# Optimization experiments

Hardware: AMD Instinct MI355X
Metric: run time of the kernel (lower is better)

## Reference

```python
import jax, jax.numpy as jnp
import numpy as np

B, DIM1, DIM2, LATENT, T = 16, 1024, 1024, 512, 2048  # T == video_feat_dim
LN_EPS = 1e-5


def setup_inputs() -> dict:
    key = jax.random.key(0)
    ks = jax.random.split(key, 8)
    def xavier(k, shape):
        fan_out, fan_in = shape
        std = float(np.sqrt(2.0 / (fan_in + fan_out)))
        return jax.random.normal(k, shape, dtype=jnp.float32) * std
    return {
        "input1": jax.random.normal(ks[0], (B, DIM1, T), dtype=jnp.float32),
        "input2": jax.random.normal(ks[1], (B, DIM2, T), dtype=jnp.float32),
        "theta_w": xavier(ks[2], (LATENT, DIM2)),
        "theta_b": jnp.zeros((LATENT,), jnp.float32),
        "phi_w": xavier(ks[3], (LATENT, DIM1)),
        "phi_b": jnp.zeros((LATENT,), jnp.float32),
        "g_w": xavier(ks[4], (LATENT, DIM1)),
        "g_b": jnp.zeros((LATENT,), jnp.float32),
        "ln_gamma": jnp.ones((LATENT, T), jnp.float32),
        "ln_beta": jnp.zeros((LATENT, T), jnp.float32),
        "out_w": xavier(ks[5], (DIM2, LATENT)),
        "out_b": jnp.zeros((DIM2,), jnp.float32),
    }


def reference(input1, input2, theta_w, theta_b, phi_w, phi_b, g_w, g_b,
              ln_gamma, ln_beta, out_w, out_b):
    # 1x1 Conv1d == channel-wise matmul
    theta_x = jnp.einsum('ld,bdt->btl', theta_w, input2) + theta_b          # [B,T2,L]
    phi_x = jnp.einsum('ld,bdt->blt', phi_w, input1) + phi_b[:, None]       # [B,L,T1]
    scores = jnp.einsum('btl,bls->bts', theta_x, phi_x)                      # [B,T2,T1] (unscaled)
    p = jax.nn.softmax(scores, axis=-1)
    g_x = jnp.einsum('ld,bdt->btl', g_w, input1) + g_b                       # [B,T1,L]
    t_x = jnp.einsum('bts,bsl->blt', p, g_x)                                 # [B,L,T2]
    # LayerNorm over the last two dims jointly [LATENT, T]
    mu = jnp.mean(t_x, axis=(1, 2), keepdims=True)
    var = jnp.var(t_x, axis=(1, 2), keepdims=True)
    h = (t_x - mu) * jax.lax.rsqrt(var + LN_EPS) * ln_gamma + ln_beta
    h = jax.nn.relu(h)
    w_t = jnp.einsum('ol,blt->bot', out_w, h) + out_b[None, :, None]         # [B,DIM2,T2]
    return w_t + input2
```

## Files before the change

### kernel.cpp

```cpp
#include <hip/hip_runtime.h>
#include <hip/hip_bf16.h>

#define BB 16
#define D1 1024
#define D2 1024
#define LL 512
#define TT 2048
#define LN_EPS 1e-5f

typedef unsigned short u16;
typedef __attribute__((ext_vector_type(8))) _Float16 half8;
typedef __attribute__((ext_vector_type(4))) float f32x4;
typedef __attribute__((ext_vector_type(4))) unsigned int u32x4;

__device__ __forceinline__ u16 f2h(float v) {
    _Float16 h = (_Float16)v;
    return *(u16*)&h;
}
__device__ __forceinline__ float h2f(u16 u) {
    return (float)(*(const _Float16*)&u);
}

__device__ __forceinline__ void gload_lds16(const void* g, void* l) {
    __builtin_amdgcn_global_load_lds((const __attribute__((address_space(1))) void*)g,
                                     (__attribute__((address_space(3))) void*)l, 16, 0, 0);
}

#define MEMFENCE asm volatile("" ::: "memory")
__device__ __forceinline__ void block_barrier() {
    MEMFENCE; __builtin_amdgcn_s_barrier(); MEMFENCE;
}

template<int BIAS, int OMODE>
__global__ __launch_bounds__(512, 1) void nt_gemm(
    const u16* __restrict__ A, const u16* __restrict__ B,
    long sAb, long sBb, long sCb,
    int N, int Kd, int gx, int gy,
    const float* __restrict__ bias,
    void* __restrict__ out0,
    const float* __restrict__ resid, long sRb)
{
    __shared__ __align__(16) u16 smem[65536];

    const int nwg = gridDim.x;
    const int id = blockIdx.x;
    const int swz = (id & 7) * (nwg >> 3) + (id >> 3);
    const int bx = swz % gx;
    const int byz = swz / gx;
    const int by = byz % gy;
    const int b = byz / gy;

    const int tid = threadIdx.x;
    const long arow0 = (long)by * 256;
    const long brow0 = (long)bx * 256;
    const u16* Ab = A + (long)b * sAb + arow0 * Kd;
    const u16* Bb = B + (long)b * sBb + brow0 * Kd;

    const int wave = tid >> 6, lane = tid & 63;
    const int mh = wave >> 2;
    const int wm = mh * 128;
    const int wn = (wave & 3) * 64;
    const int lm = lane & 15, kg = lane >> 4;

    const int ntile = Kd >> 6;

    auto STAGE = [&](int buf, long k0) {
        u16* Ad = smem + buf * 32768;
        u16* Bd = Ad + 16384;
#pragma unroll
        for (int sw = 0; sw < 4; ++sw) {
            int idx = sw * 512 + tid;
            int m = idx >> 3, s = idx & 7;
            int gs = s ^ (m & 7);
            gload_lds16(Ab + k0 + (long)m * Kd + gs * 8, Ad + idx * 8);
        }
#pragma unroll
        for (int sw = 0; sw < 4; ++sw) {
            int idx = sw * 512 + tid;
            int m = idx >> 3, s = idx & 7;
            int gs = s ^ (m & 7);
            gload_lds16(Bb + k0 + (long)m * Kd + gs * 8, Bd + idx * 8);
        }
    };

    f32x4 acc[8][4];
#pragma unroll
    for (int i = 0; i < 8; ++i)
#pragma unroll
        for (int j = 0; j < 4; ++j) acc[i][j] = (f32x4){0.f, 0.f, 0.f, 0.f};

    STAGE(0, 0);
    if (ntile > 1) STAGE(1, 64);

    half8 a_[4][2], b_[2][2];

#define LOADA(ms_) do { \
    _Pragma("unroll") for (int f = 0; f < 4; ++f) \
    _Pragma("unroll") for (int kf = 0; kf < 2; ++kf) { \
        int mr = wm + (ms_) * 64 + f * 16 + lm; \
        int ss = (kf * 4 + kg) ^ (mr & 7); \
        a_[f][kf] = *(const half8*)(Ac + mr * 64 + ss * 8); } } while (0)
#define LOADB(ns_) do { \
    _Pragma("unroll") for (int f = 0; f < 2; ++f) \
    _Pragma("unroll") for (int kf = 0; kf < 2; ++kf) { \
        int nr = wn + (ns_) * 32 + f * 16 + lm; \
        int ss = (kf * 4 + kg) ^ (nr & 7); \
        b_[f][kf] = *(const half8*)(Bc + nr * 64 + ss * 8); } } while (0)
#define PH_MFMA(ms_, ns_) do { \
    block_barrier(); \
    asm volatile("s_waitcnt lgkmcnt(0)" ::: "memory"); \
    __builtin_amdgcn_sched_barrier(0); \
    __builtin_amdgcn_s_setprio(1); \
    _Pragma("unroll") for (int i = 0; i < 4; ++i) \
    _Pragma("unroll") for (int j = 0; j < 2; ++j) \
    _Pragma("unroll") for (int kf = 0; kf < 2; ++kf) \
        acc[(ms_) * 4 + i][(ns_) * 2 + j] = __builtin_amdgcn_mfma_f32_16x16x32_f16( \
            a_[i][kf], b_[j][kf], acc[(ms_) * 4 + i][(ns_) * 2 + j], 0, 0, 0); \
    __builtin_amdgcn_s_setprio(0); \
    block_barrier(); \
} while (0)

    for (int t = 0; t < ntile; ++t) {
        const int c = t & 1;
        const u16* Ac = smem + c * 32768;
        const u16* Bc = Ac + 16384;
        if (t + 1 < ntile) { asm volatile("s_waitcnt vmcnt(8)" ::: "memory"); }
        else               { asm volatile("s_waitcnt vmcnt(0)" ::: "memory"); }
        block_barrier();

        LOADA(0); LOADB(0); PH_MFMA(0, 0);
        LOADA(1);           PH_MFMA(1, 0);
        LOADB(1);           PH_MFMA(1, 1);
        LOADA(0);           PH_MFMA(0, 1);

        if (t + 2 < ntile) STAGE(c, (long)(t + 2) * 64);
    }
#undef LOADA
#undef LOADB
#undef PH_MFMA

    float* Cs = (float*)smem;
#pragma unroll
    for (int p = 0; p < 2; ++p) {
        __syncthreads();
        if (mh == p) {
#pragma unroll
            for (int ms = 0; ms < 2; ++ms)
#pragma unroll
                for (int i = 0; i < 4; ++i)
#pragma unroll
                    for (int ns = 0; ns < 2; ++ns)
#pragma unroll
                        for (int j = 0; j < 2; ++j)
#pragma unroll
                            for (int r = 0; r < 4; ++r) {
                                int row = ms * 64 + i * 16 + kg * 4 + r;
                                int col = wn + ns * 32 + j * 16 + lm;
                                Cs[row * 256 + (col ^ ((row & 7) << 2))] = acc[ms * 4 + i][ns * 2 + j][r];
                            }
        }
        __syncthreads();
        if (OMODE == 0 || OMODE == 3) {
#pragma unroll
            for (int it = 0; it < 16; ++it) {
                int elem = it * 512 + tid;
                int row = elem >> 6, c4 = elem & 63;
                int grow = (int)arow0 + p * 128 + row;
                int gcol = (int)brow0 + c4 * 4;
                f32x4 v = *(const f32x4*)&Cs[row * 256 + ((c4 ^ (row & 7)) << 2)];
                if (BIAS == 1) v += bias[grow];
                if (BIAS == 2) v += *(const f32x4*)(bias + gcol);
                long off = (long)b * sCb + (long)grow * N + gcol;
                if (OMODE == 3) {
                    f32x4 rv = __builtin_nontemporal_load(
                        (const f32x4*)(resid + (long)b * sRb + (long)grow * N + gcol));
                    v += rv;
                    __builtin_nontemporal_store(v, (f32x4*)((float*)out0 + off));
                } else {
                    *(f32x4*)((float*)out0 + off) = v;
                }
            }
        } else {
#pragma unroll
            for (int it = 0; it < 8; ++it) {
                int elem = it * 512 + tid;
                int row = elem >> 5, c8 = elem & 31;
                int grow = (int)arow0 + p * 128 + row;
                int gcol = (int)brow0 + c8 * 8;
                int g0 = (c8 * 2) ^ (row & 7);
                int g1 = (c8 * 2 + 1) ^ (row & 7);
                f32x4 u0 = *(const f32x4*)&Cs[row * 256 + g0 * 4];
                f32x4 u1 = *(const f32x4*)&Cs[row * 256 + g1 * 4];
                float vv[8] = {u0.x, u0.y, u0.z, u0.w, u1.x, u1.y, u1.z, u1.w};
                if (BIAS == 1) {
                    float bb = bias[grow];
#pragma unroll
                    for (int q = 0; q < 8; ++q) vv[q] += bb;
                }
                if (BIAS == 2) {
#pragma unroll
                    for (int q = 0; q < 8; ++q) vv[q] += bias[gcol + q];
                }
                union { u16 u[8]; u32x4 v4; } pk;
#pragma unroll
                for (int q = 0; q < 8; ++q) pk.u[q] = f2h(vv[q]);
                long off = (long)b * sCb + (long)grow * N + gcol;
                *(u32x4*)((u16*)out0 + off) = pk.v4;
            }
        }
    }
}

__device__ __forceinline__ void stage_tile_sm(const u16* __restrict__ g, int ldk, u16* lds, int tid) {
#pragma unroll
    for (int it = 0; it < 4; ++it) {
        int idx = it * 256 + tid;
        int m = idx >> 3, s = idx & 7;
        int gs = s ^ (m & 7);
        gload_lds16(g + (long)m * ldk + gs * 8, lds + idx * 8);
    }
}

template<int BIAS, int OMODE>
__global__ __launch_bounds__(256, 4) void nt_gemm_sm(
    const u16* __restrict__ A, const u16* __restrict__ B,
    long sAb, long sBb, long sCb,
    int N, int Kd, int gx, int gy,
    const float* __restrict__ bias,
    void* __restrict__ out0,
    const float* __restrict__ resid, long sRb)
{
    __shared__ __align__(16) u16 smem[2 * 128 * 64];
    u16* As = smem;
    u16* Bs = smem + 128 * 64;

    const int nwg = gridDim.x;
    const int id = blockIdx.x;
    const int swz = (id & 7) * (nwg >> 3) + (id >> 3);
    const int bx = swz % gx;
    const int byz = swz / gx;
    const int by = byz % gy;
    const int b = byz / gy;

    const int tid = threadIdx.x;
    const long arow0 = (long)by * 128;
    const long brow0 = (long)bx * 128;
    const u16* Ab = A + (long)b * sAb + arow0 * Kd;
    const u16* Bb = B + (long)b * sBb + brow0 * Kd;

    const int wave = tid >> 6, lane = tid & 63;
    const int wm = (wave >> 1) * 64, wn = (wave & 1) * 64;
    const int lm = lane & 15, kg = lane >> 4;

    f32x4 acc[4][4];
#pragma unroll
    for (int i = 0; i < 4; ++i)
#pragma unroll
        for (int j = 0; j < 4; ++j) acc[i][j] = (f32x4){0.f, 0.f, 0.f, 0.f};

    for (int k0 = 0; k0 < Kd; k0 += 64) {
        stage_tile_sm(Ab + k0, Kd, As, tid);
        stage_tile_sm(Bb + k0, Kd, Bs, tid);
        __syncthreads();
#pragma unroll
        for (int ks = 0; ks < 2; ++ks) {
            half8 af[4], bf[4];
#pragma unroll
            for (int f = 0; f < 4; ++f) {
                int mr = wm + f * 16 + lm;
                int as_ = (ks * 4 + kg) ^ (mr & 7);
                af[f] = *(const half8*)(As + mr * 64 + as_ * 8);
                int nr = wn + f * 16 + lm;
                int bs_ = (ks * 4 + kg) ^ (nr & 7);
                bf[f] = *(const half8*)(Bs + nr * 64 + bs_ * 8);
            }
#pragma unroll
            for (int i = 0; i < 4; ++i)
#pragma unroll
                for (int j = 0; j < 4; ++j)
                    acc[i][j] = __builtin_amdgcn_mfma_f32_16x16x32_f16(af[i], bf[j], acc[i][j], 0, 0, 0);
        }
        __syncthreads();
    }

    float* Cs = (float*)smem;
#pragma unroll
    for (int p = 0; p < 2; ++p) {
        if (p) __syncthreads();
        if (wm == p * 64) {
#pragma unroll
            for (int i = 0; i < 4; ++i)
#pragma unroll
                for (int j = 0; j < 4; ++j)
#pragma unroll
                    for (int r = 0; r < 4; ++r) {
                        int row = i * 16 + kg * 4 + r;
                        int col = wn + j * 16 + lm;
                        Cs[row * 128 + (col ^ ((row & 7) << 2))] = acc[i][j][r];
                    }
        }
        __syncthreads();
        if (OMODE == 0 || OMODE == 3) {
#pragma unroll
            for (int rr = 0; rr < 8; ++rr) {
                int elem = rr * 256 + tid;
                int row = elem >> 5, c4 = elem & 31;
                int grow = (int)arow0 + p * 64 + row;
                int gcol = (int)brow0 + c4 * 4;
                f32x4 v = *(const f32x4*)&Cs[row * 128 + ((c4 ^ (row & 7)) << 2)];
                if (BIAS == 1) v += bias[grow];
                if (BIAS == 2) v += *(const f32x4*)(bias + gcol);
                long off = (long)b * sCb + (long)grow * N + gcol;
                if (OMODE == 3) {
                    f32x4 rv = __builtin_nontemporal_load(
                        (const f32x4*)(resid + (long)b * sRb + (long)grow * N + gcol));
                    v += rv;
                    __builtin_nontemporal_store(v, (f32x4*)((float*)out0 + off));
                } else {
                    *(f32x4*)((float*)out0 + off) = v;
                }
            }
        } else {
#pragma unroll
            for (int rr = 0; rr < 4; ++rr) {
                int elem = rr * 256 + tid;
                int row = elem >> 4, c8 = elem & 15;
                int grow = (int)arow0 + p * 64 + row;
                int gcol = (int)brow0 + c8 * 8;
                int g0 = (c8 * 2) ^ (row & 7);
                int g1 = (c8 * 2 + 1) ^ (row & 7);
                f32x4 u0 = *(const f32x4*)&Cs[row * 128 + g0 * 4];
                f32x4 u1 = *(const f32x4*)&Cs[row * 128 + g1 * 4];
                float vv[8] = {u0.x, u0.y, u0.z, u0.w, u1.x, u1.y, u1.z, u1.w};
                if (BIAS == 1) {
                    float bb = bias[grow];
#pragma unroll
                    for (int q = 0; q < 8; ++q) vv[q] += bb;
                }
                if (BIAS == 2) {
#pragma unroll
                    for (int q = 0; q < 8; ++q) vv[q] += bias[gcol + q];
                }
                union { u16 u[8]; u32x4 v4; } pk;
#pragma unroll
                for (int q = 0; q < 8; ++q) pk.u[q] = f2h(vv[q]);
                long off = (long)b * sCb + (long)grow * N + gcol;
                *(u32x4*)((u16*)out0 + off) = pk.v4;
            }
        }
    }
}

__global__ __launch_bounds__(256) void transpose_h(const float* __restrict__ in,
                                                   u16* __restrict__ o16, int D, int T) {
    __shared__ float tile[64][65];
    int b = blockIdx.z;
    const float* src = in + (long)b * D * T;
    long obase = (long)b * D * T;
    int t0 = blockIdx.x * 64, d0 = blockIdx.y * 64;
    int tx = threadIdx.x & 63, ty = threadIdx.x >> 6;
#pragma unroll
    for (int i = 0; i < 64; i += 4)
        tile[ty + i][tx] = __builtin_nontemporal_load(&src[(long)(d0 + ty + i) * T + t0 + tx]);
    __syncthreads();
#pragma unroll
    for (int i = 0; i < 64; i += 4) {
        long o = obase + (long)(t0 + ty + i) * D + d0 + tx;
        o16[o] = f2h(tile[tx][ty + i]);
    }
}

__global__ __launch_bounds__(256) void transpose_f32(const float* __restrict__ in,
                                                     float* __restrict__ out, int R, int C) {
    __shared__ float tile[64][65];
    int c0 = blockIdx.x * 64, r0 = blockIdx.y * 64;
    int tx = threadIdx.x & 63, ty = threadIdx.x >> 6;
#pragma unroll
    for (int i = 0; i < 64; i += 4)
        tile[ty + i][tx] = in[(long)(r0 + ty + i) * C + c0 + tx];
    __syncthreads();
#pragma unroll
    for (int i = 0; i < 64; i += 4)
        out[(long)(c0 + ty + i) * R + r0 + tx] = tile[tx][ty + i];
}

__global__ __launch_bounds__(256) void conv_w(const float* __restrict__ w,
                                              u16* __restrict__ h, int n) {
    int i = blockIdx.x * 256 + threadIdx.x;
    if (i < n) h[i] = f2h(w[i]);
}

__global__ __launch_bounds__(256) void softmax_rows(const float* __restrict__ S, u16* __restrict__ P) {
    long row = (long)blockIdx.z * TT + blockIdx.x;
    const float* s = S + row * TT;
    u16* p = P + row * TT;
    int tid = threadIdx.x;
    f32x4 v0 = *(const f32x4*)(s + tid * 8);
    f32x4 v1 = *(const f32x4*)(s + tid * 8 + 4);
    float x[8] = {v0.x, v0.y, v0.z, v0.w, v1.x, v1.y, v1.z, v1.w};
    float m = x[0];
#pragma unroll
    for (int j = 1; j < 8; ++j) m = fmaxf(m, x[j]);
#pragma unroll
    for (int off = 32; off; off >>= 1) m = fmaxf(m, __shfl_xor(m, off, 64));
    __shared__ float red[8];
    int wave = tid >> 6, lane = tid & 63;
    if (lane == 0) red[wave] = m;
    __syncthreads();
    m = fmaxf(fmaxf(red[0], red[1]), fmaxf(red[2], red[3]));
    float e[8]; float sum = 0.f;
#pragma unroll
    for (int j = 0; j < 8; ++j) { e[j] = __expf(x[j] - m); sum += e[j]; }
#pragma unroll
    for (int off = 32; off; off >>= 1) sum += __shfl_xor(sum, off, 64);
    if (lane == 0) red[4 + wave] = sum;
    __syncthreads();
    sum = red[4] + red[5] + red[6] + red[7];
    float inv = 1.f / sum;
    union { u16 u[8]; u32x4 v4; } pk;
#pragma unroll
    for (int j = 0; j < 8; ++j) pk.u[j] = f2h(e[j] * inv);
    *(u32x4*)(p + tid * 8) = pk.v4;
}

__global__ void zero32(float* p) { p[threadIdx.x] = 0.f; }

__global__ __launch_bounds__(256) void ln_partial(const u16* __restrict__ TXp, float* __restrict__ sums) {
    int b = blockIdx.z;
    const u16* x = TXp + (long)b * (LL * TT) + (long)blockIdx.x * 32768;
    int tid = threadIdx.x;
    float s = 0.f, sq = 0.f;
#pragma unroll 4
    for (int j = 0; j < 16; ++j) {
        u32x4 v = *(const u32x4*)(x + (j * 256 + tid) * 8);
        unsigned w[4] = {v.x, v.y, v.z, v.w};
#pragma unroll
        for (int q = 0; q < 4; ++q) {
            float a = h2f((u16)(w[q] & 0xffff));
            float c = h2f((u16)(w[q] >> 16));
            s += a + c;
            sq += a * a + c * c;
        }
    }
#pragma unroll
    for (int off = 32; off; off >>= 1) { s += __shfl_xor(s, off, 64); sq += __shfl_xor(sq, off, 64); }
    __shared__ float rs[8];
    int wave = tid >> 6, lane = tid & 63;
    if (lane == 0) { rs[wave] = s; rs[4 + wave] = sq; }
    __syncthreads();
    if (tid == 0) {
        atomicAdd(&sums[b * 2], rs[0] + rs[1] + rs[2] + rs[3]);
        atomicAdd(&sums[b * 2 + 1], rs[4] + rs[5] + rs[6] + rs[7]);
    }
}

__global__ __launch_bounds__(256) void ln_apply(const u16* __restrict__ TXp, const float* __restrict__ sums,
                                                const float* __restrict__ gT, const float* __restrict__ bT,
                                                u16* __restrict__ H) {
    int b = blockIdx.z;
    const float n = (float)(LL * TT);
    float mu = sums[b * 2] / n;
    float var = sums[b * 2 + 1] / n - mu * mu;
    float rstd = rsqrtf(var + LN_EPS);
    long base = (long)b * (LL * TT);
    long idx = ((long)blockIdx.x * 256 + threadIdx.x) * 8;
    u32x4 xv = *(const u32x4*)(TXp + base + idx);
    unsigned w[4] = {xv.x, xv.y, xv.z, xv.w};
    f32x4 g0 = *(const f32x4*)(gT + idx);
    f32x4 g1 = *(const f32x4*)(gT + idx + 4);
    f32x4 b0 = *(const f32x4*)(bT + idx);
    f32x4 b1 = *(const f32x4*)(bT + idx + 4);
    float g[8] = {g0.x, g0.y, g0.z, g0.w, g1.x, g1.y, g1.z, g1.w};
    float be[8] = {b0.x, b0.y, b0.z, b0.w, b1.x, b1.y, b1.z, b1.w};
    union { u16 u[8]; u32x4 v; } pk;
#pragma unroll
    for (int q = 0; q < 4; ++q) {
        float a = h2f((u16)(w[q] & 0xffff));
        float c = h2f((u16)(w[q] >> 16));
        float oa = fmaxf((a - mu) * rstd * g[q * 2] + be[q * 2], 0.f);
        float oc = fmaxf((c - mu) * rstd * g[q * 2 + 1] + be[q * 2 + 1], 0.f);
        pk.u[q * 2] = f2h(oa);
        pk.u[q * 2 + 1] = f2h(oc);
    }
    *(u32x4*)(H + base + idx) = pk.v;
}

extern "C" void kernel_launch(void* const* d_in, const int* in_sizes, int n_in,
                              void* d_out, int out_size, void* d_ws, size_t ws_size,
                              hipStream_t stream) {
    const float* input1  = (const float*)d_in[0];
    const float* input2  = (const float*)d_in[1];
    const float* theta_w = (const float*)d_in[2];
    const float* theta_b = (const float*)d_in[3];
    const float* phi_w   = (const float*)d_in[4];
    const float* phi_b   = (const float*)d_in[5];
    const float* g_w     = (const float*)d_in[6];
    const float* g_b     = (const float*)d_in[7];
    const float* ln_gamma= (const float*)d_in[8];
    const float* ln_beta = (const float*)d_in[9];
    const float* out_w   = (const float*)d_in[10];
    const float* out_b   = (const float*)d_in[11];
    float* out = (float*)d_out;

    char* ws = (char*)d_ws;
    const size_t MB = 1ull << 20;
    u16*  Xt     = (u16*)(ws + 0);
    float* scores= (float*)(ws + 0);
    u16*  pmat   = (u16*)(ws + 64 * MB);
    u16*  Qf     = (u16*)(ws + 96 * MB);
    u16*  Kf     = (u16*)(ws + 128 * MB);
    u16*  Vt     = (u16*)(ws + 160 * MB);
    u16*  TX     = (u16*)(ws + 192 * MB);
    u16*  H      = (u16*)(ws + 224 * MB);
    u16*  thw    = (u16*)(ws + 256 * MB);
    u16*  phw    = (u16*)(ws + 257 * MB);
    u16*  gww    = (u16*)(ws + 258 * MB);
    u16*  oww    = (u16*)(ws + 259 * MB);
    float* gammaT= (float*)(ws + 260 * MB);
    float* betaT = (float*)(ws + 264 * MB);
    float* sums  = (float*)(ws + 268 * MB);

    dim3 blk(256), blk5(512);

    conv_w<<<dim3((LL * D2 + 255) / 256), blk, 0, stream>>>(theta_w, thw, LL * D2);
    conv_w<<<dim3((LL * D1 + 255) / 256), blk, 0, stream>>>(phi_w, phw, LL * D1);
    conv_w<<<dim3((LL * D1 + 255) / 256), blk, 0, stream>>>(g_w, gww, LL * D1);
    conv_w<<<dim3((D2 * LL + 255) / 256), blk, 0, stream>>>(out_w, oww, D2 * LL);
    transpose_f32<<<dim3(TT / 64, LL / 64, 1), blk, 0, stream>>>(ln_gamma, gammaT, LL, TT);
    transpose_f32<<<dim3(TT / 64, LL / 64, 1), blk, 0, stream>>>(ln_beta, betaT, LL, TT);

    transpose_h<<<dim3(TT / 64, D2 / 64, BB), blk, 0, stream>>>(input2, Xt, D2, TT);
    nt_gemm_sm<2, 1><<<dim3((LL / 128) * (TT / 128) * BB), blk, 0, stream>>>(
        Xt, thw, (long)TT * D2, 0, (long)TT * LL, LL, D2, LL / 128, TT / 128,
        theta_b, Qf, nullptr, 0);

    transpose_h<<<dim3(TT / 64, D1 / 64, BB), blk, 0, stream>>>(input1, Xt, D1, TT);
    nt_gemm_sm<2, 1><<<dim3((LL / 128) * (TT / 128) * BB), blk, 0, stream>>>(
        Xt, phw, (long)TT * D1, 0, (long)TT * LL, LL, D1, LL / 128, TT / 128,
        phi_b, Kf, nullptr, 0);
    nt_gemm_sm<1, 1><<<dim3((TT / 128) * (LL / 128) * BB), blk, 0, stream>>>(
        gww, Xt, 0, (long)TT * D1, (long)LL * TT, TT, D1, TT / 128, LL / 128,
        g_b, Vt, nullptr, 0);

    for (int c = 0; c < 4; ++c) {
        long qoff = (long)c * 4 * TT * LL;
        nt_gemm<0, 0><<<dim3((TT / 256) * (TT / 256) * 4), blk5, 0, stream>>>(
            Qf + qoff, Kf + qoff, (long)TT * LL, (long)TT * LL, (long)TT * TT,
            TT, LL, TT / 256, TT / 256, nullptr, scores, nullptr, 0);
        softmax_rows<<<dim3(TT, 1, 4), blk, 0, stream>>>(scores, pmat);
        nt_gemm_sm<0, 1><<<dim3((LL / 128) * (TT / 128) * 4), blk, 0, stream>>>(
            pmat, Vt + (long)c * 4 * LL * TT, (long)TT * TT, (long)LL * TT, (long)TT * LL,
            LL, TT, LL / 128, TT / 128, nullptr, TX + qoff, nullptr, 0);
    }

    zero32<<<dim3(1), dim3(32), 0, stream>>>(sums);
    ln_partial<<<dim3(32, 1, BB), blk, 0, stream>>>(TX, sums);
    ln_apply<<<dim3(512, 1, BB), blk, 0, stream>>>(TX, sums, gammaT, betaT, H);

    nt_gemm_sm<1, 3><<<dim3((TT / 128) * (D2 / 128) * BB), blk, 0, stream>>>(
        oww, H, 0, (long)TT * LL, (long)D2 * TT, TT, LL, TT / 128, D2 / 128,
        out_b, out, input2, (long)D2 * TT);
}
```

Before: 638.4 us.

## Fuse input transpose into projection GEMMs and LayerNorm stats into PV GEMM

Replaces the separate transpose_h + half-conversion passes with a new proj_gemm that reads fp32 inputs directly from global memory, converts them to half in registers and writes transposed tiles to LDS, double-buffered with async weight loads. The PV GEMM now accumulates per-batch sum and sum of squares in its epilogue and atomically adds them, so the separate ln_partial pass over TX is removed. The nt_gemm epilogue is also trimmed to its single used mode. This avoids writing and re-reading the transposed half copies of the inputs and one full read of TX. In exchange it adds register pressure in the projection kernels and uses strided fp32 loads.

Measured after the change: 727.0 us. 13.9% more time.

```diff
diff --git a/kernel.cpp b/kernel.cpp
--- a/kernel.cpp
+++ b/kernel.cpp
@@ -160,53 +160,15 @@
                             }
         }
         __syncthreads();
-        if (OMODE == 0 || OMODE == 3) {
-#pragma unroll
-            for (int it = 0; it < 16; ++it) {
-                int elem = it * 512 + tid;
-                int row = elem >> 6, c4 = elem & 63;
-                int grow = (int)arow0 + p * 128 + row;
-                int gcol = (int)brow0 + c4 * 4;
-                f32x4 v = *(const f32x4*)&Cs[row * 256 + ((c4 ^ (row & 7)) << 2)];
-                if (BIAS == 1) v += bias[grow];
-                if (BIAS == 2) v += *(const f32x4*)(bias + gcol);
-                long off = (long)b * sCb + (long)grow * N + gcol;
-                if (OMODE == 3) {
-                    f32x4 rv = __builtin_nontemporal_load(
-                        (const f32x4*)(resid + (long)b * sRb + (long)grow * N + gcol));
-                    v += rv;
-                    __builtin_nontemporal_store(v, (f32x4*)((float*)out0 + off));
-                } else {
-                    *(f32x4*)((float*)out0 + off) = v;
-                }
-            }
-        } else {
-#pragma unroll
-            for (int it = 0; it < 8; ++it) {
-                int elem = it * 512 + tid;
-                int row = elem >> 5, c8 = elem & 31;
-                int grow = (int)arow0 + p * 128 + row;
-                int gcol = (int)brow0 + c8 * 8;
-                int g0 = (c8 * 2) ^ (row & 7);
-                int g1 = (c8 * 2 + 1) ^ (row & 7);
-                f32x4 u0 = *(const f32x4*)&Cs[row * 256 + g0 * 4];
-                f32x4 u1 = *(const f32x4*)&Cs[row * 256 + g1 * 4];
-                float vv[8] = {u0.x, u0.y, u0.z, u0.w, u1.x, u1.y, u1.z, u1.w};
-                if (BIAS == 1) {
-                    float bb = bias[grow];
-#pragma unroll
-                    for (int q = 0; q < 8; ++q) vv[q] += bb;
-                }
-                if (BIAS == 2) {
-#pragma unroll
-                    for (int q = 0; q < 8; ++q) vv[q] += bias[gcol + q];
-                }
-                union { u16 u[8]; u32x4 v4; } pk;
-#pragma unroll
-                for (int q = 0; q < 8; ++q) pk.u[q] = f2h(vv[q]);
-                long off = (long)b * sCb + (long)grow * N + gcol;
-                *(u32x4*)((u16*)out0 + off) = pk.v4;
-            }
+#pragma unroll
+        for (int it = 0; it < 16; ++it) {
+            int elem = it * 512 + tid;
+            int row = elem >> 6, c4 = elem & 63;
+            int grow = (int)arow0 + p * 128 + row;
+            int gcol = (int)brow0 + c4 * 4;
+            f32x4 v = *(const f32x4*)&Cs[row * 256 + ((c4 ^ (row & 7)) << 2)];
+            long off = (long)b * sCb + (long)grow * N + gcol;
+            *(f32x4*)((float*)out0 + off) = v;
         }
     }
 }
@@ -221,14 +183,15 @@
     }
 }
 
-template<int BIAS, int OMODE>
+template<int BIAS, int OMODE, int LNS>
 __global__ __launch_bounds__(256, 4) void nt_gemm_sm(
     const u16* __restrict__ A, const u16* __restrict__ B,
     long sAb, long sBb, long sCb,
     int N, int Kd, int gx, int gy,
     const float* __restrict__ bias,
     void* __restrict__ out0,
-    const float* __restrict__ resid, long sRb)
+    const float* __restrict__ resid, long sRb,
+    float* __restrict__ lnsums)
 {
     __shared__ __align__(16) u16 smem[2 * 128 * 64];
     u16* As = smem;
@@ -283,6 +246,7 @@
         __syncthreads();
     }
 
+    float ls = 0.f, lsq = 0.f;
     float* Cs = (float*)smem;
 #pragma unroll
     for (int p = 0; p < 2; ++p) {
@@ -341,6 +305,10 @@
 #pragma unroll
                     for (int q = 0; q < 8; ++q) vv[q] += bias[gcol + q];
                 }
+                if (LNS) {
+#pragma unroll
+                    for (int q = 0; q < 8; ++q) { ls += vv[q]; lsq += vv[q] * vv[q]; }
+                }
                 union { u16 u[8]; u32x4 v4; } pk;
 #pragma unroll
                 for (int q = 0; q < 8; ++q) pk.u[q] = f2h(vv[q]);
@@ -349,24 +317,175 @@
             }
         }
     }
-}
-
-__global__ __launch_bounds__(256) void transpose_h(const float* __restrict__ in,
-                                                   u16* __restrict__ o16, int D, int T) {
-    __shared__ float tile[64][65];
-    int b = blockIdx.z;
-    const float* src = in + (long)b * D * T;
-    long obase = (long)b * D * T;
-    int t0 = blockIdx.x * 64, d0 = blockIdx.y * 64;
-    int tx = threadIdx.x & 63, ty = threadIdx.x >> 6;
-#pragma unroll
-    for (int i = 0; i < 64; i += 4)
-        tile[ty + i][tx] = __builtin_nontemporal_load(&src[(long)(d0 + ty + i) * T + t0 + tx]);
-    __syncthreads();
-#pragma unroll
-    for (int i = 0; i < 64; i += 4) {
-        long o = obase + (long)(t0 + ty + i) * D + d0 + tx;
-        o16[o] = f2h(tile[tx][ty + i]);
+    if (LNS) {
+#pragma unroll
+        for (int off = 32; off; off >>= 1) {
+            ls += __shfl_xor(ls, off, 64);
+            lsq += __shfl_xor(lsq, off, 64);
+        }
+        __shared__ float rsum[8];
+        if (lane == 0) { rsum[wave] = ls; rsum[4 + wave] = lsq; }
+        __syncthreads();
+        if (tid == 0) {
+            atomicAdd(&lnsums[b * 2], rsum[0] + rsum[1] + rsum[2] + rsum[3]);
+            atomicAdd(&lnsums[b * 2 + 1], rsum[4] + rsum[5] + rsum[6] + rsum[7]);
+        }
+    }
+}
+
+template<int TRA, int BIAS>
+__global__ __launch_bounds__(256, 2) void proj_gemm(
+    const float* __restrict__ Xf, const u16* __restrict__ Wh,
+    long sXb, long sCb,
+    int N, int Kd, int Tt, int gx, int gy,
+    const float* __restrict__ bias,
+    u16* __restrict__ out0)
+{
+    __shared__ __align__(16) u16 smem[32768];
+
+    const int nwg = gridDim.x;
+    const int id = blockIdx.x;
+    const int swz = (id & 7) * (nwg >> 3) + (id >> 3);
+    const int bx = swz % gx;
+    const int byz = swz / gx;
+    const int by = byz % gy;
+    const int b = byz / gy;
+
+    const int tid = threadIdx.x;
+    const long arow0 = (long)by * 128;
+    const long brow0 = (long)bx * 128;
+    const long x0 = TRA ? arow0 : brow0;
+    const long wrow0 = TRA ? brow0 : arow0;
+    const float* Xb = Xf + (long)b * sXb + x0;
+    const u16* Wb = Wh + wrow0 * Kd;
+
+    const int wave = tid >> 6, lane = tid & 63;
+    const int wm = (wave >> 1) * 64, wn = (wave & 1) * 64;
+    const int lm = lane & 15, kg = lane >> 4;
+
+    const int gq = tid >> 3;
+    const int sl = tid & 7;
+
+    const int ntile = Kd >> 6;
+
+    auto WSTAGE = [&](int buf, long k0) {
+        u16* Wd = smem + 16384 + buf * 8192;
+#pragma unroll
+        for (int it = 0; it < 4; ++it) {
+            int idx = it * 256 + tid;
+            int m = idx >> 3, s = idx & 7;
+            int gs = s ^ (m & 7);
+            gload_lds16(Wb + k0 + (long)m * Kd + gs * 8, Wd + idx * 8);
+        }
+    };
+
+    f32x4 xr[8];
+    auto XLOAD = [&](long k0) {
+#pragma unroll
+        for (int r = 0; r < 8; ++r)
+            xr[r] = *(const f32x4*)(Xb + (k0 + sl * 8 + r) * Tt + gq * 4);
+    };
+    auto XWRITE = [&](int buf) {
+        u16* Xd = smem + buf * 8192;
+#pragma unroll
+        for (int j = 0; j < 4; ++j) {
+            int t = gq * 4 + j;
+            union { u16 u[8]; u32x4 v4; } pk;
+#pragma unroll
+            for (int r = 0; r < 8; ++r) pk.u[r] = f2h(xr[r][j]);
+            *(u32x4*)(Xd + t * 64 + (sl ^ (t & 7)) * 8) = pk.v4;
+        }
+    };
+
+    f32x4 acc[4][4];
+#pragma unroll
+    for (int i = 0; i < 4; ++i)
+#pragma unroll
+        for (int j = 0; j < 4; ++j) acc[i][j] = (f32x4){0.f, 0.f, 0.f, 0.f};
+
+    WSTAGE(0, 0);
+    XLOAD(0);
+
+    for (int t = 0; t < ntile; ++t) {
+        const int c = t & 1;
+        XWRITE(c);
+        if (t + 1 < ntile) {
+            WSTAGE(c ^ 1, (long)(t + 1) * 64);
+            XLOAD((long)(t + 1) * 64);
+        }
+        asm volatile("s_waitcnt lgkmcnt(0)" ::: "memory");
+        block_barrier();
+
+        const u16* Xc = smem + c * 8192;
+        const u16* Wc = smem + 16384 + c * 8192;
+        const u16* Ac = TRA ? Xc : Wc;
+        const u16* Bc = TRA ? Wc : Xc;
+#pragma unroll
+        for (int ks = 0; ks < 2; ++ks) {
+            half8 af[4], bf[4];
+#pragma unroll
+            for (int f = 0; f < 4; ++f) {
+                int mr = wm + f * 16 + lm;
+                int as_ = (ks * 4 + kg) ^ (mr & 7);
+                af[f] = *(const half8*)(Ac + mr * 64 + as_ * 8);
+                int nr = wn + f * 16 + lm;
+                int bs_ = (ks * 4 + kg) ^ (nr & 7);
+                bf[f] = *(const half8*)(Bc + nr * 64 + bs_ * 8);
+            }
+            __builtin_amdgcn_s_setprio(1);
+#pragma unroll
+            for (int i = 0; i < 4; ++i)
+#pragma unroll
+                for (int j = 0; j < 4; ++j)
+                    acc[i][j] = __builtin_amdgcn_mfma_f32_16x16x32_f16(af[i], bf[j], acc[i][j], 0, 0, 0);
+            __builtin_amdgcn_s_setprio(0);
+        }
+        block_barrier();
+    }
+
+    float* Cs = (float*)smem;
+#pragma unroll
+    for (int p = 0; p < 2; ++p) {
+        if (p) __syncthreads();
+        if (wm == p * 64) {
+#pragma unroll
+            for (int i = 0; i < 4; ++i)
+#pragma unroll
+                for (int j = 0; j < 4; ++j)
+#pragma unroll
+                    for (int r = 0; r < 4; ++r) {
+                        int row = i * 16 + kg * 4 + r;
+                        int col = wn + j * 16 + lm;
+                        Cs[row * 128 + (col ^ ((row & 7) << 2))] = acc[i][j][r];
+                    }
+        }
+        __syncthreads();
+#pragma unroll
+        for (int rr = 0; rr < 4; ++rr) {
+            int elem = rr * 256 + tid;
+            int row = elem >> 4, c8 = elem & 15;
+            int grow = (int)arow0 + p * 64 + row;
+            int gcol = (int)brow0 + c8 * 8;
+            int g0 = (c8 * 2) ^ (row & 7);
+            int g1 = (c8 * 2 + 1) ^ (row & 7);
+            f32x4 u0 = *(const f32x4*)&Cs[row * 128 + g0 * 4];
+            f32x4 u1 = *(const f32x4*)&Cs[row * 128 + g1 * 4];
+            float vv[8] = {u0.x, u0.y, u0.z, u0.w, u1.x, u1.y, u1.z, u1.w};
+            if (BIAS == 1) {
+                float bb = bias[grow];
+#pragma unroll
+                for (int q = 0; q < 8; ++q) vv[q] += bb;
+            }
+            if (BIAS == 2) {
+#pragma unroll
+                for (int q = 0; q < 8; ++q) vv[q] += bias[gcol + q];
+            }
+            union { u16 u[8]; u32x4 v4; } pk;
+#pragma unroll
+            for (int q = 0; q < 8; ++q) pk.u[q] = f2h(vv[q]);
+            long off = (long)b * sCb + (long)grow * N + gcol;
+            *(u32x4*)(out0 + off) = pk.v4;
+        }
     }
 }
 
@@ -424,35 +543,6 @@
 }
 
 __global__ void zero32(float* p) { p[threadIdx.x] = 0.f; }
-
-__global__ __launch_bounds__(256) void ln_partial(const u16* __restrict__ TXp, float* __restrict__ sums) {
-    int b = blockIdx.z;
-    const u16* x = TXp + (long)b * (LL * TT) + (long)blockIdx.x * 32768;
-    int tid = threadIdx.x;
-    float s = 0.f, sq = 0.f;
-#pragma unroll 4
-    for (int j = 0; j < 16; ++j) {
-        u32x4 v = *(const u32x4*)(x + (j * 256 + tid) * 8);
-        unsigned w[4] = {v.x, v.y, v.z, v.w};
-#pragma unroll
-        for (int q = 0; q < 4; ++q) {
-            float a = h2f((u16)(w[q] & 0xffff));
-            float c = h2f((u16)(w[q] >> 16));
-            s += a + c;
-            sq += a * a + c * c;
-        }
-    }
-#pragma unroll
-    for (int off = 32; off; off >>= 1) { s += __shfl_xor(s, off, 64); sq += __shfl_xor(sq, off, 64); }
-    __shared__ float rs[8];
-    int wave = tid >> 6, lane = tid & 63;
-    if (lane == 0) { rs[wave] = s; rs[4 + wave] = sq; }
-    __syncthreads();
-    if (tid == 0) {
-        atomicAdd(&sums[b * 2], rs[0] + rs[1] + rs[2] + rs[3]);
-        atomicAdd(&sums[b * 2 + 1], rs[4] + rs[5] + rs[6] + rs[7]);
-    }
-}
 
 __global__ __launch_bounds__(256) void ln_apply(const u16* __restrict__ TXp, const float* __restrict__ sums,
                                                 const float* __restrict__ gT, const float* __restrict__ bT,
@@ -504,7 +594,6 @@
 
     char* ws = (char*)d_ws;
     const size_t MB = 1ull << 20;
-    u16*  Xt     = (u16*)(ws + 0);
     float* scores= (float*)(ws + 0);
     u16*  pmat   = (u16*)(ws + 64 * MB);
     u16*  Qf     = (u16*)(ws + 96 * MB);
@@ -528,19 +617,17 @@
     conv_w<<<dim3((D2 * LL + 255) / 256), blk, 0, stream>>>(out_w, oww, D2 * LL);
     transpose_f32<<<dim3(TT / 64, LL / 64, 1), blk, 0, stream>>>(ln_gamma, gammaT, LL, TT);
     transpose_f32<<<dim3(TT / 64, LL / 64, 1), blk, 0, stream>>>(ln_beta, betaT, LL, TT);
-
-    transpose_h<<<dim3(TT / 64, D2 / 64, BB), blk, 0, stream>>>(input2, Xt, D2, TT);
-    nt_gemm_sm<2, 1><<<dim3((LL / 128) * (TT / 128) * BB), blk, 0, stream>>>(
-        Xt, thw, (long)TT * D2, 0, (long)TT * LL, LL, D2, LL / 128, TT / 128,
-        theta_b, Qf, nullptr, 0);
-
-    transpose_h<<<dim3(TT / 64, D1 / 64, BB), blk, 0, stream>>>(input1, Xt, D1, TT);
-    nt_gemm_sm<2, 1><<<dim3((LL / 128) * (TT / 128) * BB), blk, 0, stream>>>(
-        Xt, phw, (long)TT * D1, 0, (long)TT * LL, LL, D1, LL / 128, TT / 128,
-        phi_b, Kf, nullptr, 0);
-    nt_gemm_sm<1, 1><<<dim3((TT / 128) * (LL / 128) * BB), blk, 0, stream>>>(
-        gww, Xt, 0, (long)TT * D1, (long)LL * TT, TT, D1, TT / 128, LL / 128,
-        g_b, Vt, nullptr, 0);
+    zero32<<<dim3(1), dim3(32), 0, stream>>>(sums);
+
+    proj_gemm<1, 2><<<dim3((LL / 128) * (TT / 128) * BB), blk, 0, stream>>>(
+        input2, thw, (long)D2 * TT, (long)TT * LL, LL, D2, TT, LL / 128, TT / 128,
+        theta_b, Qf);
+    proj_gemm<1, 2><<<dim3((LL / 128) * (TT / 128) * BB), blk, 0, stream>>>(
+        input1, phw, (long)D1 * TT, (long)TT * LL, LL, D1, TT, LL / 128, TT / 128,
+        phi_b, Kf);
+    proj_gemm<0, 1><<<dim3((TT / 128) * (LL / 128) * BB), blk, 0, stream>>>(
+        input1, gww, (long)D1 * TT, (long)LL * TT, TT, D1, TT, TT / 128, LL / 128,
+        g_b, Vt);
 
     for (int c = 0; c < 4; ++c) {
         long qoff = (long)c * 4 * TT * LL;
@@ -548,16 +635,14 @@
             Qf + qoff, Kf + qoff, (long)TT * LL, (long)TT * LL, (long)TT * TT,
             TT, LL, TT / 256, TT / 256, nullptr, scores, nullptr, 0);
         softmax_rows<<<dim3(TT, 1, 4), blk, 0, stream>>>(scores, pmat);
-        nt_gemm_sm<0, 1><<<dim3((LL / 128) * (TT / 128) * 4), blk, 0, stream>>>(
+        nt_gemm_sm<0, 1, 1><<<dim3((LL / 128) * (TT / 128) * 4), blk, 0, stream>>>(
             pmat, Vt + (long)c * 4 * LL * TT, (long)TT * TT, (long)LL * TT, (long)TT * LL,
-            LL, TT, LL / 128, TT / 128, nullptr, TX + qoff, nullptr, 0);
-    }
-
-    zero32<<<dim3(1), dim3(32), 0, stream>>>(sums);
-    ln_partial<<<dim3(32, 1, BB), blk, 0, stream>>>(TX, sums);
+            LL, TT, LL / 128, TT / 128, nullptr, TX + qoff, nullptr, 0, sums + (long)c * 8);
+    }
+
     ln_apply<<<dim3(512, 1, BB), blk, 0, stream>>>(TX, sums, gammaT, betaT, H);
 
-    nt_gemm_sm<1, 3><<<dim3((TT / 128) * (D2 / 128) * BB), blk, 0, stream>>>(
+    nt_gemm_sm<1, 3, 0><<<dim3((TT / 128) * (D2 / 128) * BB), blk, 0, stream>>>(
         oww, H, 0, (long)TT * LL, (long)D2 * TT, TT, LL, TT / 128, D2 / 128,
-        out_b, out, input2, (long)D2 * TT);
-}
+        out_b, out, input2, (long)D2 * TT, nullptr);
+}
```
